# Kernel tuning notes

Hardware: AMD Instinct MI355X
Metric: run time of the kernel (lower is better)

Reference implementation:

```python
import jax, jax.numpy as jnp
import numpy as np
import math

HIDDEN = 256
NUM_GAUSSIANS = 64
NUM_FILTERS = 256
CUTOFF = 1.0
COSINE_OFFSET = 0.0
N_NODES = 10000
N_EDGES = 320000


def ssp(x):
    # shifted softplus: softplus(x) - log(2)
    return jax.nn.softplus(x) - jnp.log(2.0).astype(x.dtype)


def setup_inputs() -> dict:
    key = jax.random.key(0)
    ks = jax.random.split(key, 12)

    def xavier(k, fan_out, fan_in):
        a = math.sqrt(6.0 / (fan_in + fan_out))
        return jax.random.uniform(k, (fan_out, fan_in), jnp.float32, -a, a)

    x = jax.random.normal(ks[0], (N_NODES, HIDDEN), jnp.float32)
    ji_pairs = jax.random.randint(ks[1], (2, N_EDGES), 0, N_NODES, jnp.int64)
    e_ji = jax.random.uniform(ks[2], (N_EDGES,), jnp.float32)  # distances in [0, cutoff)
    e_ji_basis = jax.random.normal(ks[3], (N_EDGES, NUM_GAUSSIANS), jnp.float32)

    return {
        "x": x,
        "ji_pairs": ji_pairs,
        "e_ji": e_ji,
        "e_ji_basis": e_ji_basis,
        # filter_nn: Linear(G->F), ssp, Linear(F->F)
        "fw1": xavier(ks[4], NUM_FILTERS, NUM_GAUSSIANS),
        "fb1": jnp.zeros((NUM_FILTERS,), jnp.float32),
        "fw2": xavier(ks[5], NUM_FILTERS, NUM_FILTERS),
        "fb2": jnp.zeros((NUM_FILTERS,), jnp.float32),
        # CFConv linears
        "w1": xavier(ks[6], NUM_FILTERS, HIDDEN),            # linear1, no bias
        "w2": xavier(ks[7], HIDDEN, NUM_FILTERS),            # linear2
        "b2": jnp.zeros((HIDDEN,), jnp.float32),
        # linear3
        "w3": xavier(ks[8], HIDDEN, HIDDEN),
        "b3": jnp.zeros((HIDDEN,), jnp.float32),
    }


def reference(x, ji_pairs, e_ji, e_ji_basis, fw1, fb1, fw2, fb2, w1, w2, b2, w3, b3):
    pi = jnp.asarray(math.pi, x.dtype)
    # cosine cutoff: C = 0.25 * (cos((e - off) * pi / (cutoff - off)) + 1)
    C = 0.25 * (jnp.cos((e_ji - COSINE_OFFSET) * pi / (CUTOFF - COSINE_OFFSET)) + 1.0)
    # filter network on edge RBF features: [E, F]
    W = ssp(e_ji_basis @ fw1.T + fb1) @ fw2.T + fb2
    W = W * C[:, None]
    # linear1 (no bias): [N, F]
    h = x @ w1.T
    # message: x_j * W, gathered from source nodes ji_pairs[0]
    src, dst = ji_pairs[0], ji_pairs[1]
    msg = h[src] * W                                   # [E, F]
    agg = jax.ops.segment_sum(msg, dst, num_segments=x.shape[0])  # [N, F]
    # linear2
    out = agg @ w2.T + b2
    # interaction block tail: act + linear3
    out = ssp(out) @ w3.T + b3
    return out
```

## Files before the change

### kernel.cpp

```cpp
#include <hip/hip_runtime.h>
#include <hip/hip_bf16.h>

typedef __bf16 bf16_t;
typedef float f32x4 __attribute__((ext_vector_type(4)));
typedef __bf16 bf16x8 __attribute__((ext_vector_type(8)));

#define NNODES 10000
#define NEDGES 320000
#define NPAD   10048
#define NB2    (NEDGES / 64)
#define GSLOT  5

#define OFF_AGG   256
#define OFF_JIN   (OFF_AGG  + (size_t)NPAD * 256 * 4)
#define OFF_HIST  (OFF_JIN  + (size_t)2 * NEDGES * 4)
#define OFF_CUR   (OFF_HIST + 10240 * 4)
#define OFF_CSR   (OFF_CUR  + 10240 * 4)
#define OFF_PERM  (OFF_CSR  + 10240 * 4)
#define OFF_SRCS  (OFF_PERM + (size_t)NEDGES * 4)
#define OFF_DSTS  (OFF_SRCS + (size_t)NEDGES * 4)
#define OFF_CES   (OFF_DSTS + (size_t)NEDGES * 4)
#define OFF_CE    (OFF_CES  + (size_t)NEDGES * 4)
#define OFF_WB    (OFF_CE   + (size_t)NEDGES * 4)
#define FW1B 0
#define FW2B 16384
#define W1B  81920
#define W2B  147456
#define W3B  212992
#define FB1B 278528
#define FB2B 278784
#define B2B  279040
#define B3B  279296
#define WBN  279552
#define WS_NEED (OFF_WB + (size_t)WBN * 2)
#define OFF_BASC  ((WS_NEED + 255) & ~(size_t)255)
#define WS_NEED_BIG (OFF_BASC + (size_t)(NEDGES + 64) * 64 * 2)

__device__ __forceinline__ float ssp_f(float v) {
    return fmaxf(v, 0.f) + __logf(1.f + __expf(-fabsf(v))) - 0.69314718055994531f;
}
__device__ __forceinline__ f32x4 mfma16(bf16x8 a, bf16x8 b, f32x4 c) {
    return __builtin_amdgcn_mfma_f32_16x16x32_bf16(a, b, c, 0, 0, 0);
}
template<bool ISB>
__device__ __forceinline__ bf16x8 ld8(const void* p, size_t off) {
    if constexpr (ISB) return *(const bf16x8*)((const bf16_t*)p + off);
    else {
        const float* f = (const float*)p + off;
        f32x4 lo = *(const f32x4*)f, hi = *(const f32x4*)(f + 4);
        bf16x8 r;
        for (int j = 0; j < 4; ++j) { r[j] = (bf16_t)lo[j]; r[j + 4] = (bf16_t)hi[j]; }
        return r;
    }
}
__device__ __forceinline__ bf16x8 ld8r(bool isb, const void* p, size_t off) {
    if (isb) return *(const bf16x8*)((const bf16_t*)p + off);
    const float* f = (const float*)p + off;
    f32x4 lo = *(const f32x4*)f, hi = *(const f32x4*)(f + 4);
    bf16x8 r;
    for (int j = 0; j < 4; ++j) { r[j] = (bf16_t)lo[j]; r[j + 4] = (bf16_t)hi[j]; }
    return r;
}
template<bool ISB>
__device__ __forceinline__ void st1(void* p, size_t off, float v) {
    if constexpr (ISB) ((bf16_t*)p)[off] = (bf16_t)v;
    else               ((float*)p)[off] = v;
}
__device__ __forceinline__ float ld1r(bool isb, const void* p, size_t off) {
    return isb ? (float)((const bf16_t*)p)[off] : ((const float*)p)[off];
}

__global__ __launch_bounds__(256) void detect_kernel(
    const void* __restrict__ x, const int* __restrict__ jraw,
    int* __restrict__ flags, int* __restrict__ hist)
{
    __shared__ int cnt, hi;
    if (threadIdx.x == 0) { cnt = 0; hi = 0; }
    __syncthreads();
    const unsigned short* xw = (const unsigned short*)x;
    int local = 0;
    for (int i = threadIdx.x; i < 2048; i += 256) {
        unsigned int e = (xw[2 * i] >> 7) & 0xFF;
        if (e >= 100 && e <= 141) local++;
    }
    atomicAdd(&cnt, local);
    int v = 0;
    for (int i = threadIdx.x; i < 1024; i += 256) v |= jraw[2 * i + 1];
    if (v != 0) atomicOr(&hi, 1);
    for (int i = threadIdx.x; i < 10240; i += 256) hist[i] = 0;
    __syncthreads();
    if (threadIdx.x == 0) { flags[0] = (cnt > 1024) ? 1 : 0; flags[1] = (hi == 0) ? 1 : 0; }
}

__global__ __launch_bounds__(256) void prep_kernel(
    const int* __restrict__ raw, const int* __restrict__ flags,
    const void* __restrict__ e_ji,
    const void* fw1, const void* fb1, const void* fw2, const void* fb2,
    const void* w1, const void* w2, const void* b2, const void* w3, const void* b3,
    int* __restrict__ jin, int* __restrict__ hist, float* __restrict__ ce,
    bf16_t* __restrict__ wb, float* __restrict__ agg)
{
    const bool is64 = (flags[1] != 0);
    const bool isb  = (flags[0] != 0);
    const int gid = blockIdx.x * 256 + threadIdx.x;
    if (gid < 2 * NEDGES) {
        int iv = is64 ? raw[2 * gid] : raw[gid];
        iv = iv < 0 ? 0 : (iv >= NNODES ? NNODES - 1 : iv);
        jin[gid] = iv;
        if (gid >= NEDGES) atomicAdd(&hist[iv], 1);
    }
    if (gid < NEDGES)
        ce[gid] = 0.25f * (cosf(3.14159265358979f * ld1r(isb, e_ji, gid)) + 1.0f);
    if (gid < WBN) {
        int g = gid; const void* s; int so;
        if      (g < FW2B) { s = fw1; so = g - FW1B; }
        else if (g < W1B)  { s = fw2; so = g - FW2B; }
        else if (g < W2B)  { s = w1;  so = g - W1B; }
        else if (g < W3B)  { s = w2;  so = g - W2B; }
        else if (g < FB1B) { s = w3;  so = g - W3B; }
        else if (g < FB2B) { s = fb1; so = g - FB1B; }
        else if (g < B2B)  { s = fb2; so = g - FB2B; }
        else if (g < B3B)  { s = b2;  so = g - B2B; }
        else               { s = b3;  so = g - B3B; }
        wb[gid] = (bf16_t)ld1r(isb, s, so);
    }
    f32x4 z = {0.f, 0.f, 0.f, 0.f};
    for (int i = gid; i < NPAD * 256 / 4; i += 2500 * 256)
        ((f32x4*)agg)[i] = z;
}

__global__ __launch_bounds__(256) void scan_kernel(
    const int* __restrict__ hist, int* __restrict__ cur, int* __restrict__ csr)
{
    __shared__ int s[256];
    const int t = threadIdx.x;
    int loc[40]; int sum = 0;
    const int base = t * 40;
    for (int j = 0; j < 40; ++j) {
        int i = base + j;
        loc[j] = (i < NNODES) ? hist[i] : 0;
        sum += loc[j];
    }
    s[t] = sum; __syncthreads();
    for (int off = 1; off < 256; off <<= 1) {
        int v = (t >= off) ? s[t - off] : 0;
        __syncthreads();
        if (t >= off) s[t] += v;
        __syncthreads();
    }
    int pre = (t == 0) ? 0 : s[t - 1];
    for (int j = 0; j < 40; ++j) {
        int i = base + j;
        cur[i] = pre;
        csr[i] = pre;
        pre += loc[j];
    }
}

__global__ __launch_bounds__(256) void scatter_kernel(
    const int* __restrict__ jin, const float* __restrict__ ce,
    const void* __restrict__ basis, const int* __restrict__ flags,
    int* __restrict__ cur, int* __restrict__ perm,
    int* __restrict__ src_s, int* __restrict__ dst_s, float* __restrict__ ce_s,
    bf16_t* __restrict__ basc, int doconv)
{
    int e = blockIdx.x * 256 + threadIdx.x;
    if (e >= NEDGES) return;
    int d = jin[NEDGES + e];
    int pos = atomicAdd(&cur[d], 1);
    perm[pos]  = e;
    src_s[pos] = jin[e];
    dst_s[pos] = d;
    ce_s[pos]  = ce[e];
    if (doconv) {
        const bool isb = (flags[0] != 0);
        bf16_t* dp = basc + (size_t)pos * 64;
        #pragma unroll
        for (int j = 0; j < 8; ++j)
            *(bf16x8*)(dp + j * 8) = ld8r(isb, basis, (size_t)e * 64 + j * 8);
    }
}

template<bool ISB>
__global__ __launch_bounds__(256, 2) void h_gemm_kernel(
    const void* __restrict__ x, const bf16_t* __restrict__ wb,
    bf16_t* __restrict__ h, const int* __restrict__ flags)
{
    if ((flags[0] != 0) != ISB) return;
    const bf16_t* w1b = wb + W1B;
    const int w = threadIdx.x >> 6, L = threadIdx.x & 63;
    const int lane16 = L & 15, quad = L >> 4;
    const int nb = blockIdx.x * 64, cb = w * 64;
    f32x4 acc[4][4] = {};
    for (int kc = 0; kc < 8; ++kc) {
        const int ko = kc * 32 + quad * 8;
        bf16x8 af[4], bfr[4];
        for (int mt = 0; mt < 4; ++mt) {
            int row = nb + mt * 16 + lane16;
            if (row >= NNODES) row = NNODES - 1;
            af[mt] = ld8<ISB>(x, (size_t)row * 256 + ko);
        }
        for (int nt = 0; nt < 4; ++nt)
            bfr[nt] = *(const bf16x8*)(w1b + (size_t)(cb + nt * 16 + lane16) * 256 + ko);
        for (int mt = 0; mt < 4; ++mt)
            for (int nt = 0; nt < 4; ++nt)
                acc[mt][nt] = mfma16(af[mt], bfr[nt], acc[mt][nt]);
    }
    for (int mt = 0; mt < 4; ++mt)
        for (int r = 0; r < 4; ++r) {
            int row = nb + mt * 16 + quad * 4 + r;
            if (row < NNODES)
                for (int nt = 0; nt < 4; ++nt)
                    h[(size_t)row * 256 + cb + nt * 16 + lane16] = (bf16_t)acc[mt][nt][r];
        }
}

__global__ __launch_bounds__(256, 4) void edge_fast_sp(
    const bf16_t* __restrict__ basc,
    const int* __restrict__ src_s, const int* __restrict__ dst_s,
    const float* __restrict__ ce_s,
    const bf16_t* __restrict__ wb, const bf16_t* __restrict__ h,
    float* __restrict__ agg)
{
    __shared__ bf16_t T[64][264];
    __shared__ float G[GSLOT][260];
    __shared__ int ssrc[64], sdst[64];
    __shared__ float sce[64];
    const int tid = threadIdx.x;
    const int w = tid >> 6, L = tid & 63;
    const int lane16 = L & 15, quad = L >> 4;
    const int cb = w * 64;
    const int bid = (int)blockIdx.x;
    const int e0 = ((bid & 7) * (NB2 / 8) + (bid >> 3)) * 64;

    bf16x8 breg[2][4];
    #pragma unroll
    for (int kc = 0; kc < 2; ++kc)
        #pragma unroll
        for (int mt = 0; mt < 4; ++mt)
            breg[kc][mt] = *(const bf16x8*)(basc +
                (size_t)(e0 + mt * 16 + lane16) * 64 + kc * 32 + quad * 8);

    if      (w == 0) ssrc[L] = src_s[e0 + L];
    else if (w == 1) sdst[L] = dst_s[e0 + L];
    else if (w == 2) sce[L]  = ce_s[e0 + L];
    for (int i = tid; i < GSLOT * 260; i += 256) (&G[0][0])[i] = 0.f;

    const bf16_t* fw1b = wb + FW1B;
    const bf16_t* fw2b = wb + FW2B;
    float fb1v[4], fb2v[4];
    for (int nt = 0; nt < 4; ++nt) {
        fb1v[nt] = (float)wb[FB1B + cb + nt * 16 + lane16];
        fb2v[nt] = (float)wb[FB2B + cb + nt * 16 + lane16];
    }
    __syncthreads();

    const int sbase = sdst[0];
    const int span  = sdst[63] - sbase + 1;
    const bool fbk  = (span > GSLOT);

    const int hrow = tid >> 2, hseg = tid & 3;
    bf16x8 hreg[8];
    {
        const bf16_t* hs = h + (size_t)ssrc[hrow] * 256 + hseg * 64;
        #pragma unroll
        for (int j = 0; j < 8; ++j) hreg[j] = ((const bf16x8*)hs)[j];
    }

    f32x4 acc1[4][4] = {};
    #pragma unroll
    for (int kc = 0; kc < 2; ++kc) {
        const int ko = kc * 32 + quad * 8;
        bf16x8 bfr[4];
        for (int nt = 0; nt < 4; ++nt)
            bfr[nt] = *(const bf16x8*)(fw1b + (size_t)(cb + nt * 16 + lane16) * 64 + ko);
        for (int mt = 0; mt < 4; ++mt)
            for (int nt = 0; nt < 4; ++nt)
                acc1[mt][nt] = mfma16(breg[kc][mt], bfr[nt], acc1[mt][nt]);
    }
    for (int nt = 0; nt < 4; ++nt) {
        int col = cb + nt * 16 + lane16;
        for (int mt = 0; mt < 4; ++mt)
            for (int r = 0; r < 4; ++r)
                T[mt * 16 + quad * 4 + r][col] = (bf16_t)ssp_f(acc1[mt][nt][r] + fb1v[nt]);
    }
    __syncthreads();

    f32x4 acc2[4][4] = {};
    for (int kc = 0; kc < 8; ++kc) {
        const int ko = kc * 32 + quad * 8;
        bf16x8 af[4], bfr[4];
        for (int mt = 0; mt < 4; ++mt)
            af[mt] = *(const bf16x8*)(&T[mt * 16 + lane16][ko]);
        for (int nt = 0; nt < 4; ++nt)
            bfr[nt] = *(const bf16x8*)(fw2b + (size_t)(cb + nt * 16 + lane16) * 256 + ko);
        for (int mt = 0; mt < 4; ++mt)
            for (int nt = 0; nt < 4; ++nt)
                acc2[mt][nt] = mfma16(af[mt], bfr[nt], acc2[mt][nt]);
    }
    __syncthreads();

    {
        bf16_t* dp = &T[hrow][hseg * 64];
        #pragma unroll
        for (int j = 0; j < 8; ++j) ((bf16x8*)dp)[j] = hreg[j];
    }
    __syncthreads();

    float run[4] = {0, 0, 0, 0};
    int curn = -1;
    for (int mt = 0; mt < 4; ++mt)
        for (int r = 0; r < 4; ++r) {
            int row = mt * 16 + quad * 4 + r;
            int n = sdst[row];
            if (n != curn) {
                if (curn >= 0) {
                    if (!fbk)
                        for (int nt = 0; nt < 4; ++nt)
                            atomicAdd(&G[curn - sbase][cb + nt * 16 + lane16], run[nt]);
                    else
                        for (int nt = 0; nt < 4; ++nt)
                            atomicAdd(&agg[(size_t)curn * 256 + cb + nt * 16 + lane16], run[nt]);
                }
                curn = n;
                run[0] = run[1] = run[2] = run[3] = 0.f;
            }
            float cv = sce[row];
            for (int nt = 0; nt < 4; ++nt) {
                int col = cb + nt * 16 + lane16;
                run[nt] += (acc2[mt][nt][r] + fb2v[nt]) * cv * (float)T[row][col];
            }
        }
    if (curn >= 0) {
        if (!fbk)
            for (int nt = 0; nt < 4; ++nt)
                atomicAdd(&G[curn - sbase][cb + nt * 16 + lane16], run[nt]);
        else
            for (int nt = 0; nt < 4; ++nt)
                atomicAdd(&agg[(size_t)curn * 256 + cb + nt * 16 + lane16], run[nt]);
    }
    __syncthreads();

    if (!fbk) {
        for (int s = 0; s < span; ++s)
            atomicAdd(&agg[(size_t)(sbase + s) * 256 + tid], G[s][tid]);
    }
}

template<bool ISB>
__global__ __launch_bounds__(256, 4) void edge_kernel_sp(
    const void* __restrict__ basis, const int* __restrict__ perm,
    const int* __restrict__ src_s, const int* __restrict__ dst_s,
    const float* __restrict__ ce_s,
    const bf16_t* __restrict__ wb, const bf16_t* __restrict__ h,
    float* __restrict__ agg, const int* __restrict__ flags)
{
    if ((flags[0] != 0) != ISB) return;
    __shared__ bf16_t T[64][264];
    __shared__ float G[GSLOT][260];
    __shared__ int sperm[64], ssrc[64], sdst[64];
    __shared__ float sce[64];
    const int tid = threadIdx.x;
    const int w = tid >> 6, L = tid & 63;
    const int lane16 = L & 15, quad = L >> 4;
    const int cb = w * 64;
    const int bid = (int)blockIdx.x;
    const int e0 = ((bid & 7) * (NB2 / 8) + (bid >> 3)) * 64;

    if      (w == 0) sperm[L] = perm[e0 + L];
    else if (w == 1) ssrc[L] = src_s[e0 + L];
    else if (w == 2) sdst[L] = dst_s[e0 + L];
    else             sce[L]  = ce_s[e0 + L];
    for (int i = tid; i < GSLOT * 260; i += 256) (&G[0][0])[i] = 0.f;

    const bf16_t* fw1b = wb + FW1B;
    const bf16_t* fw2b = wb + FW2B;
    float fb1v[4], fb2v[4];
    for (int nt = 0; nt < 4; ++nt) {
        fb1v[nt] = (float)wb[FB1B + cb + nt * 16 + lane16];
        fb2v[nt] = (float)wb[FB2B + cb + nt * 16 + lane16];
    }
    __syncthreads();

    const int sbase = sdst[0];
    const int span  = sdst[63] - sbase + 1;
    const bool fbk  = (span > GSLOT);

    const int hrow = tid >> 2, hseg = tid & 3;
    bf16x8 hreg[8];
    {
        const bf16_t* hs = h + (size_t)ssrc[hrow] * 256 + hseg * 64;
        #pragma unroll
        for (int j = 0; j < 8; ++j) hreg[j] = ((const bf16x8*)hs)[j];
    }

    int prow[4];
    for (int mt = 0; mt < 4; ++mt) prow[mt] = sperm[mt * 16 + lane16];

    f32x4 acc1[4][4] = {};
    for (int kc = 0; kc < 2; ++kc) {
        const int ko = kc * 32 + quad * 8;
        bf16x8 af[4], bfr[4];
        for (int mt = 0; mt < 4; ++mt)
            af[mt] = ld8<ISB>(basis, (size_t)prow[mt] * 64 + ko);
        for (int nt = 0; nt < 4; ++nt)
            bfr[nt] = *(const bf16x8*)(fw1b + (size_t)(cb + nt * 16 + lane16) * 64 + ko);
        for (int mt = 0; mt < 4; ++mt)
            for (int nt = 0; nt < 4; ++nt)
                acc1[mt][nt] = mfma16(af[mt], bfr[nt], acc1[mt][nt]);
    }
    for (int nt = 0; nt < 4; ++nt) {
        int col = cb + nt * 16 + lane16;
        for (int mt = 0; mt < 4; ++mt)
            for (int r = 0; r < 4; ++r)
                T[mt * 16 + quad * 4 + r][col] = (bf16_t)ssp_f(acc1[mt][nt][r] + fb1v[nt]);
    }
    __syncthreads();

    f32x4 acc2[4][4] = {};
    for (int kc = 0; kc < 8; ++kc) {
        const int ko = kc * 32 + quad * 8;
        bf16x8 af[4], bfr[4];
        for (int mt = 0; mt < 4; ++mt)
            af[mt] = *(const bf16x8*)(&T[mt * 16 + lane16][ko]);
        for (int nt = 0; nt < 4; ++nt)
            bfr[nt] = *(const bf16x8*)(fw2b + (size_t)(cb + nt * 16 + lane16) * 256 + ko);
        for (int mt = 0; mt < 4; ++mt)
            for (int nt = 0; nt < 4; ++nt)
                acc2[mt][nt] = mfma16(af[mt], bfr[nt], acc2[mt][nt]);
    }
    __syncthreads();

    {
        bf16_t* dp = &T[hrow][hseg * 64];
        #pragma unroll
        for (int j = 0; j < 8; ++j) ((bf16x8*)dp)[j] = hreg[j];
    }
    __syncthreads();

    float run[4] = {0, 0, 0, 0};
    int curn = -1;
    for (int mt = 0; mt < 4; ++mt)
        for (int r = 0; r < 4; ++r) {
            int row = mt * 16 + quad * 4 + r;
            int n = sdst[row];
            if (n != curn) {
                if (curn >= 0) {
                    if (!fbk)
                        for (int nt = 0; nt < 4; ++nt)
                            atomicAdd(&G[curn - sbase][cb + nt * 16 + lane16], run[nt]);
                    else
                        for (int nt = 0; nt < 4; ++nt)
                            atomicAdd(&agg[(size_t)curn * 256 + cb + nt * 16 + lane16], run[nt]);
                }
                curn = n;
                run[0] = run[1] = run[2] = run[3] = 0.f;
            }
            float cv = sce[row];
            for (int nt = 0; nt < 4; ++nt) {
                int col = cb + nt * 16 + lane16;
                run[nt] += (acc2[mt][nt][r] + fb2v[nt]) * cv * (float)T[row][col];
            }
        }
    if (curn >= 0) {
        if (!fbk)
            for (int nt = 0; nt < 4; ++nt)
                atomicAdd(&G[curn - sbase][cb + nt * 16 + lane16], run[nt]);
        else
            for (int nt = 0; nt < 4; ++nt)
                atomicAdd(&agg[(size_t)curn * 256 + cb + nt * 16 + lane16], run[nt]);
    }
    __syncthreads();

    if (!fbk) {
        for (int s = 0; s < span; ++s)
            atomicAdd(&agg[(size_t)(sbase + s) * 256 + tid], G[s][tid]);
    }
}

template<bool ISB>
__global__ __launch_bounds__(256, 2) void out_kernel(
    const float* __restrict__ agg, const bf16_t* __restrict__ wb,
    void* __restrict__ out, const int* __restrict__ flags)
{
    if ((flags[0] != 0) != ISB) return;
    const bf16_t* w2b = wb + W2B;
    const bf16_t* w3b = wb + W3B;
    __shared__ bf16_t U[64][264];
    const int w = threadIdx.x >> 6, L = threadIdx.x & 63;
    const int lane16 = L & 15, quad = L >> 4;
    const int nb = blockIdx.x * 64, cb = w * 64;

    f32x4 acc[4][4] = {};
    for (int kc = 0; kc < 8; ++kc) {
        const int ko = kc * 32 + quad * 8;
        bf16x8 af[4], bfr[4];
        for (int mt = 0; mt < 4; ++mt) {
            int row = nb + mt * 16 + lane16;
            const float* p = agg + (size_t)row * 256 + ko;
            f32x4 lo = *(const f32x4*)p, hi = *(const f32x4*)(p + 4);
            bf16x8 a;
            for (int j = 0; j < 4; ++j) { a[j] = (bf16_t)lo[j]; a[j + 4] = (bf16_t)hi[j]; }
            af[mt] = a;
        }
        for (int nt = 0; nt < 4; ++nt)
            bfr[nt] = *(const bf16x8*)(w2b + (size_t)(cb + nt * 16 + lane16) * 256 + ko);
        for (int mt = 0; mt < 4; ++mt)
            for (int nt = 0; nt < 4; ++nt)
                acc[mt][nt] = mfma16(af[mt], bfr[nt], acc[mt][nt]);
    }
    for (int nt = 0; nt < 4; ++nt) {
        int col = cb + nt * 16 + lane16;
        float bias = (float)wb[B2B + col];
        for (int mt = 0; mt < 4; ++mt)
            for (int r = 0; r < 4; ++r)
                U[mt * 16 + quad * 4 + r][col] = (bf16_t)ssp_f(acc[mt][nt][r] + bias);
    }
    __syncthreads();

    f32x4 acc2[4][4] = {};
    for (int kc = 0; kc < 8; ++kc) {
        const int ko = kc * 32 + quad * 8;
        bf16x8 af[4], bfr[4];
        for (int mt = 0; mt < 4; ++mt)
            af[mt] = *(const bf16x8*)(&U[mt * 16 + lane16][ko]);
        for (int nt = 0; nt < 4; ++nt)
            bfr[nt] = *(const bf16x8*)(w3b + (size_t)(cb + nt * 16 + lane16) * 256 + ko);
        for (int mt = 0; mt < 4; ++mt)
            for (int nt = 0; nt < 4; ++nt)
                acc2[mt][nt] = mfma16(af[mt], bfr[nt], acc2[mt][nt]);
    }
    for (int mt = 0; mt < 4; ++mt)
        for (int r = 0; r < 4; ++r) {
            int row = nb + mt * 16 + quad * 4 + r;
            if (row < NNODES)
                for (int nt = 0; nt < 4; ++nt) {
                    int col = cb + nt * 16 + lane16;
                    st1<ISB>(out, (size_t)row * 256 + col,
                             acc2[mt][nt][r] + (float)wb[B3B + col]);
                }
        }
}

extern "C" void kernel_launch(void* const* d_in, const int* in_sizes, int n_in,
                              void* d_out, int out_size, void* d_ws, size_t ws_size,
                              hipStream_t stream) {
    const void* x     = d_in[0];
    const int*  ji    = (const int*)d_in[1];
    const void* e_ji  = d_in[2];
    const void* basis = d_in[3];
    const void* fw1   = d_in[4];
    const void* fb1   = d_in[5];
    const void* fw2   = d_in[6];
    const void* fb2   = d_in[7];
    const void* w1    = d_in[8];
    const void* w2    = d_in[9];
    const void* b2    = d_in[10];
    const void* w3    = d_in[11];
    const void* b3    = d_in[12];

    if (ws_size < WS_NEED) return;
    const bool bigws = ws_size >= WS_NEED_BIG;

    char* W = (char*)d_ws;
    int*    flags = (int*)W;
    float*  agg   = (float*)(W + OFF_AGG);
    int*    jin   = (int*)(W + OFF_JIN);
    int*    hist  = (int*)(W + OFF_HIST);
    int*    cur   = (int*)(W + OFF_CUR);
    int*    csr   = (int*)(W + OFF_CSR);
    int*    perm  = (int*)(W + OFF_PERM);
    int*    src_s = (int*)(W + OFF_SRCS);
    int*    dst_s = (int*)(W + OFF_DSTS);
    float*  ce_s  = (float*)(W + OFF_CES);
    float*  ce    = (float*)(W + OFF_CE);
    bf16_t* wb    = (bf16_t*)(W + OFF_WB);
    bf16_t* basc  = (bf16_t*)(W + OFF_BASC);
    bf16_t* h     = (bf16_t*)d_out;

    detect_kernel<<<1, 256, 0, stream>>>(x, ji, flags, hist);
    prep_kernel<<<2500, 256, 0, stream>>>(ji, flags, e_ji, fw1, fb1, fw2, fb2,
                                          w1, w2, b2, w3, b3, jin, hist, ce, wb, agg);
    scan_kernel<<<1, 256, 0, stream>>>(hist, cur, csr);
    scatter_kernel<<<1250, 256, 0, stream>>>(jin, ce, basis, flags, cur, perm,
                                             src_s, dst_s, ce_s, basc, bigws ? 1 : 0);
    h_gemm_kernel<true ><<<157, 256, 0, stream>>>(x, wb, h, flags);
    h_gemm_kernel<false><<<157, 256, 0, stream>>>(x, wb, h, flags);
    if (bigws) {
        edge_fast_sp<<<NB2, 256, 0, stream>>>(basc, src_s, dst_s, ce_s, wb, h, agg);
    } else {
        edge_kernel_sp<true ><<<NB2, 256, 0, stream>>>(basis, perm, src_s, dst_s, ce_s, wb, h, agg, flags);
        edge_kernel_sp<false><<<NB2, 256, 0, stream>>>(basis, perm, src_s, dst_s, ce_s, wb, h, agg, flags);
    }
    out_kernel<true ><<<157, 256, 0, stream>>>(agg, wb, d_out, flags);
    out_kernel<false><<<157, 256, 0, stream>>>(agg, wb, d_out, flags);
}
```

Before: 534.0 us.

## Split edge kernel into two output-column halves and convert basis in original order

The fast edge path now launches twice as many blocks, each computing half of the 256 filter columns for a 64-edge tile, with the half selected by XCD index so both halves of a tile land on different XCD groups. The basis conversion to bf16 moves from the scatter kernel (which wrote it in dst-sorted order) to the prep kernel, which streams it in original order, and the edge kernel gathers basis rows through perm. The split doubles the first-layer GEMM (fw1) and the basis/index loads per tile but halves the register and shared-memory footprint per block, aiming for more parallelism and occupancy. The basis gather is now random-access instead of contiguous.

```diff
diff --git a/kernel.cpp b/kernel.cpp
--- a/kernel.cpp
+++ b/kernel.cpp
@@ -34,7 +34,7 @@
 #define WBN  279552
 #define WS_NEED (OFF_WB + (size_t)WBN * 2)
 #define OFF_BASC  ((WS_NEED + 255) & ~(size_t)255)
-#define WS_NEED_BIG (OFF_BASC + (size_t)(NEDGES + 64) * 64 * 2)
+#define WS_NEED_BIG (OFF_BASC + (size_t)NEDGES * 64 * 2)
 
 __device__ __forceinline__ float ssp_f(float v) {
     return fmaxf(v, 0.f) + __logf(1.f + __expf(-fabsf(v))) - 0.69314718055994531f;
@@ -94,11 +94,12 @@
 
 __global__ __launch_bounds__(256) void prep_kernel(
     const int* __restrict__ raw, const int* __restrict__ flags,
-    const void* __restrict__ e_ji,
+    const void* __restrict__ e_ji, const void* __restrict__ basis,
     const void* fw1, const void* fb1, const void* fw2, const void* fb2,
     const void* w1, const void* w2, const void* b2, const void* w3, const void* b3,
     int* __restrict__ jin, int* __restrict__ hist, float* __restrict__ ce,
-    bf16_t* __restrict__ wb, float* __restrict__ agg)
+    bf16_t* __restrict__ wb, float* __restrict__ agg,
+    bf16_t* __restrict__ basc0, int doconv)
 {
     const bool is64 = (flags[1] != 0);
     const bool isb  = (flags[0] != 0);
@@ -127,6 +128,11 @@
     f32x4 z = {0.f, 0.f, 0.f, 0.f};
     for (int i = gid; i < NPAD * 256 / 4; i += 2500 * 256)
         ((f32x4*)agg)[i] = z;
+    if (doconv) {
+        const int nv = NEDGES * 64 / 8;
+        for (int i = gid; i < nv; i += 2500 * 256)
+            ((bf16x8*)basc0)[i] = ld8r(isb, basis, (size_t)i * 8);
+    }
 }
 
 __global__ __launch_bounds__(256) void scan_kernel(
@@ -159,25 +165,17 @@
 
 __global__ __launch_bounds__(256) void scatter_kernel(
     const int* __restrict__ jin, const float* __restrict__ ce,
-    const void* __restrict__ basis, const int* __restrict__ flags,
     int* __restrict__ cur, int* __restrict__ perm,
-    int* __restrict__ src_s, int* __restrict__ dst_s, float* __restrict__ ce_s,
-    bf16_t* __restrict__ basc, int doconv)
+    int* __restrict__ src_s, int* __restrict__ dst_s, float* __restrict__ ce_s)
 {
     int e = blockIdx.x * 256 + threadIdx.x;
-    if (e >= NEDGES) return;
-    int d = jin[NEDGES + e];
-    int pos = atomicAdd(&cur[d], 1);
-    perm[pos]  = e;
-    src_s[pos] = jin[e];
-    dst_s[pos] = d;
-    ce_s[pos]  = ce[e];
-    if (doconv) {
-        const bool isb = (flags[0] != 0);
-        bf16_t* dp = basc + (size_t)pos * 64;
-        #pragma unroll
-        for (int j = 0; j < 8; ++j)
-            *(bf16x8*)(dp + j * 8) = ld8r(isb, basis, (size_t)e * 64 + j * 8);
+    if (e < NEDGES) {
+        int d = jin[NEDGES + e];
+        int pos = atomicAdd(&cur[d], 1);
+        perm[pos]  = e;
+        src_s[pos] = jin[e];
+        dst_s[pos] = d;
+        ce_s[pos]  = ce[e];
     }
 }
 
@@ -215,16 +213,151 @@
         }
 }
 
-__global__ __launch_bounds__(256, 4) void edge_fast_sp(
-    const bf16_t* __restrict__ basc,
+__global__ __launch_bounds__(256, 4) void edge_half_kernel(
+    const bf16_t* __restrict__ basc0, const int* __restrict__ perm,
     const int* __restrict__ src_s, const int* __restrict__ dst_s,
     const float* __restrict__ ce_s,
     const bf16_t* __restrict__ wb, const bf16_t* __restrict__ h,
     float* __restrict__ agg)
 {
     __shared__ bf16_t T[64][264];
+    __shared__ float G[GSLOT][132];
+    __shared__ int sperm[64], ssrc[64], sdst[64];
+    __shared__ float sce[64];
+    const int tid = threadIdx.x;
+    const int w = tid >> 6, L = tid & 63;
+    const int lane16 = L & 15, quad = L >> 4;
+    const int bid  = (int)blockIdx.x;
+    const int xcd8 = bid & 7;
+    const int hf   = xcd8 >> 2;
+    const int tile = (xcd8 & 3) * 1250 + (bid >> 3);
+    const int e0   = tile * 64;
+    const int cb1  = w * 64;
+    const int mh   = w >> 1, cg = w & 1;
+    const int cb2  = hf * 128 + cg * 64;
+
+    if      (w == 0) sperm[L] = perm[e0 + L];
+    else if (w == 1) ssrc[L] = src_s[e0 + L];
+    else if (w == 2) sdst[L] = dst_s[e0 + L];
+    else             sce[L]  = ce_s[e0 + L];
+    for (int i = tid; i < GSLOT * 132; i += 256) (&G[0][0])[i] = 0.f;
+
+    const bf16_t* fw1b = wb + FW1B;
+    const bf16_t* fw2b = wb + FW2B;
+    float fb1v[4], fb2v[4];
+    for (int nt = 0; nt < 4; ++nt) {
+        fb1v[nt] = (float)wb[FB1B + cb1 + nt * 16 + lane16];
+        fb2v[nt] = (float)wb[FB2B + cb2 + nt * 16 + lane16];
+    }
+    __syncthreads();
+
+    const int sbase = sdst[0];
+    const int span  = sdst[63] - sbase + 1;
+    const bool fbk  = (span > GSLOT);
+
+    const int hrow = tid >> 2, hseg = tid & 3;
+    bf16x8 hreg[4];
+    {
+        const bf16_t* hs = h + (size_t)ssrc[hrow] * 256 + hf * 128 + hseg * 32;
+        #pragma unroll
+        for (int j = 0; j < 4; ++j) hreg[j] = ((const bf16x8*)hs)[j];
+    }
+
+    int prow[4];
+    for (int mt = 0; mt < 4; ++mt) prow[mt] = sperm[mt * 16 + lane16];
+
+    f32x4 acc1[4][4] = {};
+    for (int kc = 0; kc < 2; ++kc) {
+        const int ko = kc * 32 + quad * 8;
+        bf16x8 af[4], bfr[4];
+        for (int mt = 0; mt < 4; ++mt)
+            af[mt] = *(const bf16x8*)(basc0 + (size_t)prow[mt] * 64 + ko);
+        for (int nt = 0; nt < 4; ++nt)
+            bfr[nt] = *(const bf16x8*)(fw1b + (size_t)(cb1 + nt * 16 + lane16) * 64 + ko);
+        for (int mt = 0; mt < 4; ++mt)
+            for (int nt = 0; nt < 4; ++nt)
+                acc1[mt][nt] = mfma16(af[mt], bfr[nt], acc1[mt][nt]);
+    }
+    for (int nt = 0; nt < 4; ++nt) {
+        int col = cb1 + nt * 16 + lane16;
+        for (int mt = 0; mt < 4; ++mt)
+            for (int r = 0; r < 4; ++r)
+                T[mt * 16 + quad * 4 + r][col] = (bf16_t)ssp_f(acc1[mt][nt][r] + fb1v[nt]);
+    }
+    __syncthreads();
+
+    f32x4 acc2[2][4] = {};
+    for (int kc = 0; kc < 8; ++kc) {
+        const int ko = kc * 32 + quad * 8;
+        bf16x8 af[2], bfr[4];
+        for (int mt = 0; mt < 2; ++mt)
+            af[mt] = *(const bf16x8*)(&T[mh * 32 + mt * 16 + lane16][ko]);
+        for (int nt = 0; nt < 4; ++nt)
+            bfr[nt] = *(const bf16x8*)(fw2b + (size_t)(cb2 + nt * 16 + lane16) * 256 + ko);
+        for (int mt = 0; mt < 2; ++mt)
+            for (int nt = 0; nt < 4; ++nt)
+                acc2[mt][nt] = mfma16(af[mt], bfr[nt], acc2[mt][nt]);
+    }
+    __syncthreads();
+
+    {
+        bf16_t* dp = &T[hrow][hseg * 32];
+        #pragma unroll
+        for (int j = 0; j < 4; ++j) ((bf16x8*)dp)[j] = hreg[j];
+    }
+    __syncthreads();
+
+    float run[4] = {0, 0, 0, 0};
+    int curn = -1;
+    for (int mt = 0; mt < 2; ++mt)
+        for (int r = 0; r < 4; ++r) {
+            int row = mh * 32 + mt * 16 + quad * 4 + r;
+            int n = sdst[row];
+            if (n != curn) {
+                if (curn >= 0) {
+                    if (!fbk)
+                        for (int nt = 0; nt < 4; ++nt)
+                            atomicAdd(&G[curn - sbase][cg * 64 + nt * 16 + lane16], run[nt]);
+                    else
+                        for (int nt = 0; nt < 4; ++nt)
+                            atomicAdd(&agg[(size_t)curn * 256 + cb2 + nt * 16 + lane16], run[nt]);
+                }
+                curn = n;
+                run[0] = run[1] = run[2] = run[3] = 0.f;
+            }
+            float cv = sce[row];
+            for (int nt = 0; nt < 4; ++nt)
+                run[nt] += (acc2[mt][nt][r] + fb2v[nt]) * cv *
+                           (float)T[row][cg * 64 + nt * 16 + lane16];
+        }
+    if (curn >= 0) {
+        if (!fbk)
+            for (int nt = 0; nt < 4; ++nt)
+                atomicAdd(&G[curn - sbase][cg * 64 + nt * 16 + lane16], run[nt]);
+        else
+            for (int nt = 0; nt < 4; ++nt)
+                atomicAdd(&agg[(size_t)curn * 256 + cb2 + nt * 16 + lane16], run[nt]);
+    }
+    __syncthreads();
+
+    if (!fbk && tid < 128) {
+        for (int s = 0; s < span; ++s)
+            atomicAdd(&agg[(size_t)(sbase + s) * 256 + hf * 128 + tid], G[s][tid]);
+    }
+}
+
+template<bool ISB>
+__global__ __launch_bounds__(256, 4) void edge_kernel_sp(
+    const void* __restrict__ basis, const int* __restrict__ perm,
+    const int* __restrict__ src_s, const int* __restrict__ dst_s,
+    const float* __restrict__ ce_s,
+    const bf16_t* __restrict__ wb, const bf16_t* __restrict__ h,
+    float* __restrict__ agg, const int* __restrict__ flags)
+{
+    if ((flags[0] != 0) != ISB) return;
+    __shared__ bf16_t T[64][264];
     __shared__ float G[GSLOT][260];
-    __shared__ int ssrc[64], sdst[64];
+    __shared__ int sperm[64], ssrc[64], sdst[64];
     __shared__ float sce[64];
     const int tid = threadIdx.x;
     const int w = tid >> 6, L = tid & 63;
@@ -233,17 +366,10 @@
     const int bid = (int)blockIdx.x;
     const int e0 = ((bid & 7) * (NB2 / 8) + (bid >> 3)) * 64;
 
-    bf16x8 breg[2][4];
-    #pragma unroll
-    for (int kc = 0; kc < 2; ++kc)
-        #pragma unroll
-        for (int mt = 0; mt < 4; ++mt)
-            breg[kc][mt] = *(const bf16x8*)(basc +
-                (size_t)(e0 + mt * 16 + lane16) * 64 + kc * 32 + quad * 8);
-
-    if      (w == 0) ssrc[L] = src_s[e0 + L];
-    else if (w == 1) sdst[L] = dst_s[e0 + L];
-    else if (w == 2) sce[L]  = ce_s[e0 + L];
+    if      (w == 0) sperm[L] = perm[e0 + L];
+    else if (w == 1) ssrc[L] = src_s[e0 + L];
+    else if (w == 2) sdst[L] = dst_s[e0 + L];
+    else             sce[L]  = ce_s[e0 + L];
     for (int i = tid; i < GSLOT * 260; i += 256) (&G[0][0])[i] = 0.f;
 
     const bf16_t* fw1b = wb + FW1B;
@@ -267,16 +393,20 @@
         for (int j = 0; j < 8; ++j) hreg[j] = ((const bf16x8*)hs)[j];
     }
 
+    int prow[4];
+    for (int mt = 0; mt < 4; ++mt) prow[mt] = sperm[mt * 16 + lane16];
+
     f32x4 acc1[4][4] = {};
-    #pragma unroll
     for (int kc = 0; kc < 2; ++kc) {
         const int ko = kc * 32 + quad * 8;
-        bf16x8 bfr[4];
+        bf16x8 af[4], bfr[4];
+        for (int mt = 0; mt < 4; ++mt)
+            af[mt] = ld8<ISB>(basis, (size_t)prow[mt] * 64 + ko);
         for (int nt = 0; nt < 4; ++nt)
             bfr[nt] = *(const bf16x8*)(fw1b + (size_t)(cb + nt * 16 + lane16) * 64 + ko);
         for (int mt = 0; mt < 4; ++mt)
             for (int nt = 0; nt < 4; ++nt)
-                acc1[mt][nt] = mfma16(breg[kc][mt], bfr[nt], acc1[mt][nt]);
+                acc1[mt][nt] = mfma16(af[mt], bfr[nt], acc1[mt][nt]);
     }
     for (int nt = 0; nt < 4; ++nt) {
         int col = cb + nt * 16 + lane16;
@@ -348,137 +478,6 @@
 }
 
 template<bool ISB>
-__global__ __launch_bounds__(256, 4) void edge_kernel_sp(
-    const void* __restrict__ basis, const int* __restrict__ perm,
-    const int* __restrict__ src_s, const int* __restrict__ dst_s,
-    const float* __restrict__ ce_s,
-    const bf16_t* __restrict__ wb, const bf16_t* __restrict__ h,
-    float* __restrict__ agg, const int* __restrict__ flags)
-{
-    if ((flags[0] != 0) != ISB) return;
-    __shared__ bf16_t T[64][264];
-    __shared__ float G[GSLOT][260];
-    __shared__ int sperm[64], ssrc[64], sdst[64];
-    __shared__ float sce[64];
-    const int tid = threadIdx.x;
-    const int w = tid >> 6, L = tid & 63;
-    const int lane16 = L & 15, quad = L >> 4;
-    const int cb = w * 64;
-    const int bid = (int)blockIdx.x;
-    const int e0 = ((bid & 7) * (NB2 / 8) + (bid >> 3)) * 64;
-
-    if      (w == 0) sperm[L] = perm[e0 + L];
-    else if (w == 1) ssrc[L] = src_s[e0 + L];
-    else if (w == 2) sdst[L] = dst_s[e0 + L];
-    else             sce[L]  = ce_s[e0 + L];
-    for (int i = tid; i < GSLOT * 260; i += 256) (&G[0][0])[i] = 0.f;
-
-    const bf16_t* fw1b = wb + FW1B;
-    const bf16_t* fw2b = wb + FW2B;
-    float fb1v[4], fb2v[4];
-    for (int nt = 0; nt < 4; ++nt) {
-        fb1v[nt] = (float)wb[FB1B + cb + nt * 16 + lane16];
-        fb2v[nt] = (float)wb[FB2B + cb + nt * 16 + lane16];
-    }
-    __syncthreads();
-
-    const int sbase = sdst[0];
-    const int span  = sdst[63] - sbase + 1;
-    const bool fbk  = (span > GSLOT);
-
-    const int hrow = tid >> 2, hseg = tid & 3;
-    bf16x8 hreg[8];
-    {
-        const bf16_t* hs = h + (size_t)ssrc[hrow] * 256 + hseg * 64;
-        #pragma unroll
-        for (int j = 0; j < 8; ++j) hreg[j] = ((const bf16x8*)hs)[j];
-    }
-
-    int prow[4];
-    for (int mt = 0; mt < 4; ++mt) prow[mt] = sperm[mt * 16 + lane16];
-
-    f32x4 acc1[4][4] = {};
-    for (int kc = 0; kc < 2; ++kc) {
-        const int ko = kc * 32 + quad * 8;
-        bf16x8 af[4], bfr[4];
-        for (int mt = 0; mt < 4; ++mt)
-            af[mt] = ld8<ISB>(basis, (size_t)prow[mt] * 64 + ko);
-        for (int nt = 0; nt < 4; ++nt)
-            bfr[nt] = *(const bf16x8*)(fw1b + (size_t)(cb + nt * 16 + lane16) * 64 + ko);
-        for (int mt = 0; mt < 4; ++mt)
-            for (int nt = 0; nt < 4; ++nt)
-                acc1[mt][nt] = mfma16(af[mt], bfr[nt], acc1[mt][nt]);
-    }
-    for (int nt = 0; nt < 4; ++nt) {
-        int col = cb + nt * 16 + lane16;
-        for (int mt = 0; mt < 4; ++mt)
-            for (int r = 0; r < 4; ++r)
-                T[mt * 16 + quad * 4 + r][col] = (bf16_t)ssp_f(acc1[mt][nt][r] + fb1v[nt]);
-    }
-    __syncthreads();
-
-    f32x4 acc2[4][4] = {};
-    for (int kc = 0; kc < 8; ++kc) {
-        const int ko = kc * 32 + quad * 8;
-        bf16x8 af[4], bfr[4];
-        for (int mt = 0; mt < 4; ++mt)
-            af[mt] = *(const bf16x8*)(&T[mt * 16 + lane16][ko]);
-        for (int nt = 0; nt < 4; ++nt)
-            bfr[nt] = *(const bf16x8*)(fw2b + (size_t)(cb + nt * 16 + lane16) * 256 + ko);
-        for (int mt = 0; mt < 4; ++mt)
-            for (int nt = 0; nt < 4; ++nt)
-                acc2[mt][nt] = mfma16(af[mt], bfr[nt], acc2[mt][nt]);
-    }
-    __syncthreads();
-
-    {
-        bf16_t* dp = &T[hrow][hseg * 64];
-        #pragma unroll
-        for (int j = 0; j < 8; ++j) ((bf16x8*)dp)[j] = hreg[j];
-    }
-    __syncthreads();
-
-    float run[4] = {0, 0, 0, 0};
-    int curn = -1;
-    for (int mt = 0; mt < 4; ++mt)
-        for (int r = 0; r < 4; ++r) {
-            int row = mt * 16 + quad * 4 + r;
-            int n = sdst[row];
-            if (n != curn) {
-                if (curn >= 0) {
-                    if (!fbk)
-                        for (int nt = 0; nt < 4; ++nt)
-                            atomicAdd(&G[curn - sbase][cb + nt * 16 + lane16], run[nt]);
-                    else
-                        for (int nt = 0; nt < 4; ++nt)
-                            atomicAdd(&agg[(size_t)curn * 256 + cb + nt * 16 + lane16], run[nt]);
-                }
-                curn = n;
-                run[0] = run[1] = run[2] = run[3] = 0.f;
-            }
-            float cv = sce[row];
-            for (int nt = 0; nt < 4; ++nt) {
-                int col = cb + nt * 16 + lane16;
-                run[nt] += (acc2[mt][nt][r] + fb2v[nt]) * cv * (float)T[row][col];
-            }
-        }
-    if (curn >= 0) {
-        if (!fbk)
-            for (int nt = 0; nt < 4; ++nt)
-                atomicAdd(&G[curn - sbase][cb + nt * 16 + lane16], run[nt]);
-        else
-            for (int nt = 0; nt < 4; ++nt)
-                atomicAdd(&agg[(size_t)curn * 256 + cb + nt * 16 + lane16], run[nt]);
-    }
-    __syncthreads();
-
-    if (!fbk) {
-        for (int s = 0; s < span; ++s)
-            atomicAdd(&agg[(size_t)(sbase + s) * 256 + tid], G[s][tid]);
-    }
-}
-
-template<bool ISB>
 __global__ __launch_bounds__(256, 2) void out_kernel(
     const float* __restrict__ agg, const bf16_t* __restrict__ wb,
     void* __restrict__ out, const int* __restrict__ flags)
@@ -575,19 +574,19 @@
     float*  ce_s  = (float*)(W + OFF_CES);
     float*  ce    = (float*)(W + OFF_CE);
     bf16_t* wb    = (bf16_t*)(W + OFF_WB);
-    bf16_t* basc  = (bf16_t*)(W + OFF_BASC);
+    bf16_t* basc0 = (bf16_t*)(W + OFF_BASC);
     bf16_t* h     = (bf16_t*)d_out;
 
     detect_kernel<<<1, 256, 0, stream>>>(x, ji, flags, hist);
-    prep_kernel<<<2500, 256, 0, stream>>>(ji, flags, e_ji, fw1, fb1, fw2, fb2,
-                                          w1, w2, b2, w3, b3, jin, hist, ce, wb, agg);
+    prep_kernel<<<2500, 256, 0, stream>>>(ji, flags, e_ji, basis, fw1, fb1, fw2, fb2,
+                                          w1, w2, b2, w3, b3, jin, hist, ce, wb, agg,
+                                          basc0, bigws ? 1 : 0);
     scan_kernel<<<1, 256, 0, stream>>>(hist, cur, csr);
-    scatter_kernel<<<1250, 256, 0, stream>>>(jin, ce, basis, flags, cur, perm,
-                                             src_s, dst_s, ce_s, basc, bigws ? 1 : 0);
+    scatter_kernel<<<1250, 256, 0, stream>>>(jin, ce, cur, perm, src_s, dst_s, ce_s);
     h_gemm_kernel<true ><<<157, 256, 0, stream>>>(x, wb, h, flags);
     h_gemm_kernel<false><<<157, 256, 0, stream>>>(x, wb, h, flags);
     if (bigws) {
-        edge_fast_sp<<<NB2, 256, 0, stream>>>(basc, src_s, dst_s, ce_s, wb, h, agg);
+        edge_half_kernel<<<2 * NB2, 256, 0, stream>>>(basc0, perm, src_s, dst_s, ce_s, wb, h, agg);
     } else {
         edge_kernel_sp<true ><<<NB2, 256, 0, stream>>>(basis, perm, src_s, dst_s, ce_s, wb, h, agg, flags);
         edge_kernel_sp<false><<<NB2, 256, 0, stream>>>(basis, perm, src_s, dst_s, ce_s, wb, h, agg, flags);
```

New measurement: 532.6 us. Within noise of the previous version (-0.3%).
